# Kernel tuning notes

Hardware: AMD Instinct MI355X
Metric: run time of the kernel (lower is better)

Reference implementation:

```python
import jax, jax.numpy as jnp
import numpy as np

V, S, D, H = 32000, 1024, 768, 3072
EPS = 1e-5


def pos_encoding(seq_len, dim, dtype=jnp.float32):
    # pe[pos, i] = sin(pos/10000^(i/dim)) if i even else cos(pos/10000^(i/dim))
    pos = jnp.arange(seq_len, dtype=dtype)[:, None]
    i = jnp.arange(dim, dtype=dtype)[None, :]
    ang = pos / jnp.power(jnp.asarray(10000.0, dtype), i / dim)
    even = (jnp.arange(dim) % 2 == 0)[None, :]
    return jnp.where(even, jnp.sin(ang), jnp.cos(ang))


def layernorm2d(x, w, b):
    # normalizes over last two dims (token_size, input_dim), affine params [S, D]
    m = jnp.mean(x, axis=(-2, -1), keepdims=True)
    v = jnp.mean((x - m) ** 2, axis=(-2, -1), keepdims=True)
    return (x - m) / jnp.sqrt(v + EPS) * w + b


def setup_inputs() -> dict:
    key = jax.random.key(0)
    ks = jax.random.split(key, 16)
    sc = 0.02
    emb = jax.random.normal(ks[0], (V, D), jnp.float32) * sc
    emb = emb.at[0].set(0.0)  # padding_idx=0
    inp = {
        "x": jax.random.randint(ks[1], (8, S), 0, V),
        "emb": emb,
        "Wq": jax.random.normal(ks[2], (D, H), jnp.float32) * sc,
        "bq": jnp.zeros((H,), jnp.float32),
        "Wk": jax.random.normal(ks[3], (D, H), jnp.float32) * sc,
        "bk": jnp.zeros((H,), jnp.float32),
        "Wv": jax.random.normal(ks[4], (D, H), jnp.float32) * sc,
        "bv": jnp.zeros((H,), jnp.float32),
        "Wo": jax.random.normal(ks[5], (H, D), jnp.float32) * sc,
        "bo": jnp.zeros((D,), jnp.float32),
        "W1": jax.random.normal(ks[6], (D, H), jnp.float32) * sc,
        "b1": jnp.zeros((H,), jnp.float32),
        "W2": jax.random.normal(ks[7], (H, D), jnp.float32) * sc,
        "b2": jnp.zeros((D,), jnp.float32),
        "ln1_w": jnp.ones((S, D), jnp.float32),
        "ln1_b": jnp.zeros((S, D), jnp.float32),
        "ln2_w": jnp.ones((S, D), jnp.float32),
        "ln2_b": jnp.zeros((S, D), jnp.float32),
    }
    return inp


def reference(x, emb, Wq, bq, Wk, bk, Wv, bv, Wo, bo, W1, b1, W2, b2, ln1_w, ln1_b, ln2_w, ln2_b):
    y = emb[x]                                   # [B, S, D]
    y = y + pos_encoding(y.shape[1], y.shape[2], y.dtype)
    # unscaled self-attention (no 1/sqrt(d) factor, faithful to source)
    q = y @ Wq + bq
    k = y @ Wk + bk
    v = y @ Wv + bv
    attn = jax.nn.softmax(jnp.einsum("bsh,bth->bst", q, k), axis=-1)
    a = jnp.einsum("bst,bth->bsh", attn, v) @ Wo + bo
    y = layernorm2d(y + a, ln1_w, ln1_b)
    # FFN: GELU applied AFTER second linear (faithful to source)
    f = jax.nn.gelu((y @ W1 + b1) @ W2 + b2, approximate=False)
    y = layernorm2d(y + f, ln2_w, ln2_b)
    return y
```

## Files before the change

kernel.cpp:

```cpp
#include <hip/hip_runtime.h>
#include <hip/hip_fp16.h>

#define DI __device__ __forceinline__

typedef _Float16 f16x8 __attribute__((ext_vector_type(8)));
typedef float f32x4 __attribute__((ext_vector_type(4)));

struct alignas(8) h4 { __half x, y, z, w; };

DI float waveReduceSum(float v) {
#pragma unroll
  for (int i = 1; i < 64; i <<= 1) v += __shfl_xor(v, i);
  return v;
}
DI float waveReduceMax(float v) {
#pragma unroll
  for (int i = 1; i < 64; i <<= 1) v = fmaxf(v, __shfl_xor(v, i));
  return v;
}

DI float gelu_exact(float x) { return 0.5f * x * (1.f + erff(x * 0.70710678118654752f)); }

#define MFMA16(b_, a_, c_) __builtin_amdgcn_mfma_f32_16x16x32_f16((b_), (a_), (c_), 0, 0, 0)

template <typename CT, bool BIAS, bool BROW>
__global__ __launch_bounds__(512, 2) void gemm_nt8(
    const __half* __restrict__ A, int lda, long long sA,
    const __half* __restrict__ Bt, int ldb, long long sB,
    const float* __restrict__ bias, long long sBias,
    CT* __restrict__ C, int ldc, long long sC,
    int nT, int K) {
  __shared__ __align__(16) __half As[2][16384];
  __shared__ __align__(16) __half Bs[2][16384];

  const int tid = threadIdx.x;
  const int wave = tid >> 6, lane = tid & 63;

  const int gsz = 4 * nT;
  const int g = blockIdx.x / gsz, r = blockIdx.x % gsz;
  const int m0 = (g * 4 + (r & 3)) * 256;
  const int n0 = (r >> 2) * 256;

  A += (long long)blockIdx.z * sA;
  Bt += (long long)blockIdx.z * sB;
  C += (long long)blockIdx.z * sC;
  if constexpr (BIAS || BROW) bias += (long long)blockIdx.z * sBias;

  const int wm = wave >> 2, wn = wave & 3;

  f32x4 acc[8][4];
#pragma unroll
  for (int i = 0; i < 8; ++i)
#pragma unroll
    for (int j = 0; j < 4; ++j) acc[i][j] = (f32x4){0.f, 0.f, 0.f, 0.f};

  const int srow = tid >> 3;
  const int gc = (tid & 7) ^ (srow & 7);
  const __half* Ag = A + (size_t)(m0 + srow) * lda + gc * 8;
  const __half* Bg = Bt + (size_t)(n0 + srow) * ldb + gc * 8;
  const size_t a64 = (size_t)64 * lda, b64 = (size_t)64 * ldb;
  char* AsWr = (char*)As + tid * 16;
  char* BsWr = (char*)Bs + tid * 16;

  f16x8 sra[4], srb[4];

#define LDG(t)                                                        \
  {                                                                   \
    const __half* sa_ = Ag + (t) * 64;                                \
    const __half* sb_ = Bg + (t) * 64;                                \
    sra[0] = *(const f16x8*)(sa_);                                    \
    sra[1] = *(const f16x8*)(sa_ + a64);                              \
    sra[2] = *(const f16x8*)(sa_ + 2 * a64);                          \
    sra[3] = *(const f16x8*)(sa_ + 3 * a64);                          \
    srb[0] = *(const f16x8*)(sb_);                                    \
    srb[1] = *(const f16x8*)(sb_ + b64);                              \
    srb[2] = *(const f16x8*)(sb_ + 2 * b64);                          \
    srb[3] = *(const f16x8*)(sb_ + 3 * b64);                          \
  }
#define DSW(t)                                                        \
  {                                                                   \
    char* da_ = AsWr + (((t) & 1) ? 32768 : 0);                       \
    char* db_ = BsWr + (((t) & 1) ? 32768 : 0);                       \
    *(f16x8*)(da_) = sra[0];                                          \
    *(f16x8*)(da_ + 8192) = sra[1];                                   \
    *(f16x8*)(da_ + 16384) = sra[2];                                  \
    *(f16x8*)(da_ + 24576) = sra[3];                                  \
    *(f16x8*)(db_) = srb[0];                                          \
    *(f16x8*)(db_ + 8192) = srb[1];                                   \
    *(f16x8*)(db_ + 16384) = srb[2];                                  \
    *(f16x8*)(db_ + 24576) = srb[3];                                  \
  }

  const int ml = lane & 15, q = lane >> 4, lx = lane & 7;
  const int co0 = (q ^ lx) * 16, co1 = co0 ^ 64;
  const char* Ar = (const char*)As + wm * 16384 + ml * 128;
  const char* Br = (const char*)Bs + (wn >> 1) * 16384 + (wn & 1) * 8192 + ml * 128;

  const int nt = K >> 6;
  LDG(0);
  DSW(0);
  if (nt > 1) LDG(1);
  asm volatile("s_waitcnt lgkmcnt(0)" ::: "memory");
  __builtin_amdgcn_s_barrier();
  __builtin_amdgcn_sched_barrier(0);

  for (int t = 0; t < nt; ++t) {
    if (t + 1 < nt) {
      DSW(t + 1);
      if (t + 2 < nt) LDG(t + 2);
    }
    const int pb = (t & 1) ? 32768 : 0;
    const char* Ap = Ar + pb;
    const char* Bp = Br + pb;
    f16x8 af[8], bf[4];
#pragma unroll
    for (int ks = 0; ks < 2; ++ks) {
      const int co = ks ? co1 : co0;
#pragma unroll
      for (int i = 0; i < 8; ++i) af[i] = *(const f16x8*)(Ap + i * 2048 + co);
#pragma unroll
      for (int j = 0; j < 4; ++j) bf[j] = *(const f16x8*)(Bp + j * 2048 + co);
#pragma unroll
      for (int i = 0; i < 8; ++i)
#pragma unroll
        for (int j = 0; j < 4; ++j)
          acc[i][j] = MFMA16(bf[j], af[i], acc[i][j]);
    }
    asm volatile("s_waitcnt lgkmcnt(0)" ::: "memory");
    __builtin_amdgcn_s_barrier();
    __builtin_amdgcn_sched_barrier(0);
  }
#undef LDG
#undef DSW

#pragma unroll
  for (int j = 0; j < 4; ++j) {
    const int col0 = n0 + wn * 64 + j * 16 + q * 4;
    float4 bc = {0.f, 0.f, 0.f, 0.f};
    if constexpr (BIAS) bc = *(const float4*)(bias + col0);
#pragma unroll
    for (int i = 0; i < 8; ++i) {
      const int row = m0 + wm * 128 + i * 16 + ml;
      const float br = BROW ? bias[row] : 0.f;
      const float v0 = acc[i][j][0] + bc.x + br;
      const float v1 = acc[i][j][1] + bc.y + br;
      const float v2 = acc[i][j][2] + bc.z + br;
      const float v3 = acc[i][j][3] + bc.w + br;
      if constexpr (sizeof(CT) == 4) {
        *(float4*)(C + (size_t)row * ldc + col0) = make_float4(v0, v1, v2, v3);
      } else {
        h4 o{__float2half(v0), __float2half(v1), __float2half(v2), __float2half(v3)};
        *(h4*)((__half*)C + (size_t)row * ldc + col0) = o;
      }
    }
  }
}

template <typename CT, bool BIAS, bool BROW>
__global__ __launch_bounds__(256, 2) void gemm_nt(
    const __half* __restrict__ A, int lda, long long sA,
    const __half* __restrict__ Bt, int ldb, long long sB,
    const float* __restrict__ bias, long long sBias,
    CT* __restrict__ C, int ldc, long long sC,
    int nT, int K) {
  __shared__ __align__(16) __half As[2][8192];
  __shared__ __align__(16) __half Bs[2][8192];

  const int tid = threadIdx.x;
  const int wave = tid >> 6, lane = tid & 63;

  const int gsz = 8 * nT;
  const int g = blockIdx.x / gsz, r = blockIdx.x % gsz;
  const int m0 = (g * 8 + (r & 7)) * 128;
  const int n0 = (r >> 3) * 128;

  A += (long long)blockIdx.z * sA;
  Bt += (long long)blockIdx.z * sB;
  C += (long long)blockIdx.z * sC;
  if constexpr (BIAS || BROW) bias += (long long)blockIdx.z * sBias;
  const int wm = wave & 1, wn = wave >> 1;

  f32x4 acc[4][4];
#pragma unroll
  for (int i = 0; i < 4; ++i)
#pragma unroll
    for (int jj = 0; jj < 4; ++jj) acc[i][jj] = (f32x4){0.f, 0.f, 0.f, 0.f};

  const int srow = tid >> 3;
  const int gc = (tid & 7) ^ (srow & 7);
  const __half* Ag = A + (size_t)(m0 + srow) * lda + gc * 8;
  const __half* Bg = Bt + (size_t)(n0 + srow) * ldb + gc * 8;
  const size_t a32 = (size_t)32 * lda, b32 = (size_t)32 * ldb;
  char* AsWr = (char*)As + tid * 16;
  char* BsWr = (char*)Bs + tid * 16;

  f16x8 sra[4], srb[4];

#define LDG(t)                                                        \
  {                                                                   \
    const __half* sa_ = Ag + (t) * 64;                                \
    const __half* sb_ = Bg + (t) * 64;                                \
    sra[0] = *(const f16x8*)(sa_);                                    \
    sra[1] = *(const f16x8*)(sa_ + a32);                              \
    sra[2] = *(const f16x8*)(sa_ + 2 * a32);                          \
    sra[3] = *(const f16x8*)(sa_ + 3 * a32);                          \
    srb[0] = *(const f16x8*)(sb_);                                    \
    srb[1] = *(const f16x8*)(sb_ + b32);                              \
    srb[2] = *(const f16x8*)(sb_ + 2 * b32);                          \
    srb[3] = *(const f16x8*)(sb_ + 3 * b32);                          \
  }
#define DSW(t)                                                        \
  {                                                                   \
    char* da_ = AsWr + (((t) & 1) ? 16384 : 0);                       \
    char* db_ = BsWr + (((t) & 1) ? 16384 : 0);                       \
    *(f16x8*)(da_) = sra[0];                                          \
    *(f16x8*)(da_ + 4096) = sra[1];                                   \
    *(f16x8*)(da_ + 8192) = sra[2];                                   \
    *(f16x8*)(da_ + 12288) = sra[3];                                  \
    *(f16x8*)(db_) = srb[0];                                          \
    *(f16x8*)(db_ + 4096) = srb[1];                                   \
    *(f16x8*)(db_ + 8192) = srb[2];                                   \
    *(f16x8*)(db_ + 12288) = srb[3];                                  \
  }

  const int ml = lane & 15, q = lane >> 4, lx = lane & 7;
  const int aoff = ((wm * 64 + ml) * 8 + (q ^ lx)) * 16;
  const int boff = ((wn * 64 + ml) * 8 + (q ^ lx)) * 16;

  const int nt = K >> 6;
  LDG(0);
  DSW(0);
  if (nt > 1) LDG(1);
  asm volatile("s_waitcnt lgkmcnt(0)" ::: "memory");
  __builtin_amdgcn_s_barrier();
  __builtin_amdgcn_sched_barrier(0);

  for (int t = 0; t < nt; ++t) {
    if (t + 1 < nt) {
      DSW(t + 1);
      if (t + 2 < nt) LDG(t + 2);
    }
    const int pb = (t & 1) ? 16384 : 0;
#pragma unroll
    for (int jj = 0; jj < 2; ++jj) {
      const char* Ab = (const char*)As + pb + (jj ? (aoff ^ 64) : aoff);
      const char* Bb = (const char*)Bs + pb + (jj ? (boff ^ 64) : boff);
      f16x8 af[4], bf[4];
#pragma unroll
      for (int i = 0; i < 4; ++i) {
        af[i] = *(const f16x8*)(Ab + i * 2048);
        bf[i] = *(const f16x8*)(Bb + i * 2048);
      }
#pragma unroll
      for (int i = 0; i < 4; ++i)
#pragma unroll
        for (int jn = 0; jn < 4; ++jn)
          acc[i][jn] = MFMA16(bf[jn], af[i], acc[i][jn]);
    }
    asm volatile("s_waitcnt lgkmcnt(0)" ::: "memory");
    __builtin_amdgcn_s_barrier();
    __builtin_amdgcn_sched_barrier(0);
  }
#undef LDG
#undef DSW

#pragma unroll
  for (int jn = 0; jn < 4; ++jn) {
    const int col0 = n0 + wn * 64 + jn * 16 + q * 4;
    float4 bc = {0.f, 0.f, 0.f, 0.f};
    if constexpr (BIAS) bc = *(const float4*)(bias + col0);
#pragma unroll
    for (int i = 0; i < 4; ++i) {
      const int row = m0 + wm * 64 + i * 16 + ml;
      const float br = BROW ? bias[row] : 0.f;
      const float v0 = acc[i][jn][0] + bc.x + br;
      const float v1 = acc[i][jn][1] + bc.y + br;
      const float v2 = acc[i][jn][2] + bc.z + br;
      const float v3 = acc[i][jn][3] + bc.w + br;
      if constexpr (sizeof(CT) == 4) {
        *(float4*)(C + (size_t)row * ldc + col0) = make_float4(v0, v1, v2, v3);
      } else {
        h4 o{__float2half(v0), __float2half(v1), __float2half(v2), __float2half(v3)};
        *(h4*)((__half*)C + (size_t)row * ldc + col0) = o;
      }
    }
  }
}

__global__ __launch_bounds__(256) void prep(
    const float* __restrict__ Wq, const float* __restrict__ Wk,
    const float* __restrict__ Wv, const float* __restrict__ W1,
    const float* __restrict__ Wo, const float* __restrict__ W2,
    const float* __restrict__ bq, const float* __restrict__ bk,
    __half* __restrict__ wD, __half* __restrict__ wB, __half* __restrict__ wC,
    __half* __restrict__ wA, float* __restrict__ bqk) {
  if (blockIdx.x == 2304) {
    if (blockIdx.y == 0)
      for (int i = threadIdx.x; i < 3072; i += 256) {
        bqk[i] = bq[i];
        bqk[3072 + i] = bk[i];
      }
    return;
  }
  __shared__ float t[32][33];
  const int tx = threadIdx.x & 31, ty = threadIdx.x >> 5;
  if (blockIdx.y < 4) {
    const float* in;
    __half* out;
    switch (blockIdx.y) {
      case 0: in = Wq; out = wD; break;
      case 1: in = Wk; out = wD + 3072 * 768; break;
      case 2: in = Wv; out = wB; break;
      default: in = W1; out = wC; break;
    }
    const int cb = blockIdx.x % 96, rb = blockIdx.x / 96;
    const int c = cb * 32 + tx, r0 = rb * 32;
#pragma unroll
    for (int i = 0; i < 32; i += 8) t[ty + i][tx] = in[(size_t)(r0 + ty + i) * 3072 + c];
    __syncthreads();
    const int oc = r0 + tx, o0 = cb * 32;
#pragma unroll
    for (int i = 0; i < 32; i += 8)
      out[(size_t)(o0 + ty + i) * 768 + oc] = __float2half(t[tx][ty + i]);
  } else {
    const float* in = (blockIdx.y == 5) ? W2 : Wo;
    __half* out = wA + ((blockIdx.y == 5) ? 3072 * 768 : 0);
    const int cb = blockIdx.x % 24, rb = blockIdx.x / 24;
    const int c = cb * 32 + tx, r0 = rb * 32;
#pragma unroll
    for (int i = 0; i < 32; i += 8) t[ty + i][tx] = in[(size_t)(r0 + ty + i) * 768 + c];
    __syncthreads();
    const int oc = r0 + tx, o0 = cb * 32;
#pragma unroll
    for (int i = 0; i < 32; i += 8)
      out[(size_t)(o0 + ty + i) * 3072 + oc] = __float2half(t[tx][ty + i]);
  }
}

__global__ __launch_bounds__(256) void embed_pos_kernel(
    const int* __restrict__ x, const float* __restrict__ emb,
    float* __restrict__ y, __half* __restrict__ yh) {
  const int row = blockIdx.x;
  const int s = row & 1023;
  const int tok = x[row];
  const float* ep = emb + (size_t)tok * 768;
  float* yp = y + (size_t)row * 768;
  __half* hp = yh + (size_t)row * 768;
  const float c = -13.287712379549449f / 768.f;
  for (int d = threadIdx.x; d < 768; d += 256) {
    float ang = (float)s * exp2f((float)d * c);
    float pe = (d & 1) ? cosf(ang) : sinf(ang);
    float v = ep[d] + pe;
    yp[d] = v;
    hp[d] = __float2half(v);
  }
}

__global__ __launch_bounds__(256) void softmax_rows(
    const float* __restrict__ L, __half* __restrict__ P) {
  const size_t row = blockIdx.x;
  const float4 x = ((const float4*)(L + row * 1024))[threadIdx.x];
  const int wave = threadIdx.x >> 6, lane = threadIdx.x & 63;
  float m = fmaxf(fmaxf(x.x, x.y), fmaxf(x.z, x.w));
  m = waveReduceMax(m);
  __shared__ float sm[4];
  __shared__ float ssum[4];
  if (lane == 0) sm[wave] = m;
  __syncthreads();
  m = fmaxf(fmaxf(sm[0], sm[1]), fmaxf(sm[2], sm[3]));
  float e0 = expf(x.x - m), e1 = expf(x.y - m), e2 = expf(x.z - m), e3 = expf(x.w - m);
  float s = e0 + e1 + e2 + e3;
  s = waveReduceSum(s);
  if (lane == 0) ssum[wave] = s;
  __syncthreads();
  s = ssum[0] + ssum[1] + ssum[2] + ssum[3];
  const float inv = 1.f / s;
  h4 o{__float2half(e0 * inv), __float2half(e1 * inv), __float2half(e2 * inv),
       __float2half(e3 * inv)};
  ((h4*)(P + row * 1024))[threadIdx.x] = o;
}

template <bool GELU>
__global__ __launch_bounds__(256) void residual_stats(
    float* __restrict__ y, const float* __restrict__ p0, const float* __restrict__ p1,
    const float* __restrict__ bias, float2* __restrict__ partials) {
  const int b = blockIdx.y, chunk = blockIdx.x;
  const size_t base = (size_t)b * 786432 + (size_t)chunk * 8192;
  float4* yp = (float4*)(y + base);
  const float4* a0 = (const float4*)(p0 + base);
  const float4* a1 = (const float4*)(p1 + base);
  float s = 0.f, ss = 0.f;
#pragma unroll
  for (int it = 0; it < 8; ++it) {
    const int idx = it * 256 + threadIdx.x;
    const int d = (chunk * 8192 + it * 1024 + threadIdx.x * 4) % 768;
    float4 yv = yp[idx];
    float4 v0 = a0[idx];
    float4 v1 = a1[idx];
    const float4 bv = *(const float4*)(bias + d);
    float ax = v0.x + v1.x + bv.x, ay = v0.y + v1.y + bv.y;
    float az = v0.z + v1.z + bv.z, aw = v0.w + v1.w + bv.w;
    if constexpr (GELU) {
      ax = gelu_exact(ax); ay = gelu_exact(ay);
      az = gelu_exact(az); aw = gelu_exact(aw);
    }
    float4 r{yv.x + ax, yv.y + ay, yv.z + az, yv.w + aw};
    yp[idx] = r;
    s += r.x + r.y + r.z + r.w;
    ss += r.x * r.x + r.y * r.y + r.z * r.z + r.w * r.w;
  }
  s = waveReduceSum(s);
  ss = waveReduceSum(ss);
  __shared__ float2 wr[4];
  const int wave = threadIdx.x >> 6, lane = threadIdx.x & 63;
  if (lane == 0) wr[wave] = make_float2(s, ss);
  __syncthreads();
  if (threadIdx.x == 0) {
    float S = wr[0].x + wr[1].x + wr[2].x + wr[3].x;
    float SS = wr[0].y + wr[1].y + wr[2].y + wr[3].y;
    partials[b * 96 + chunk] = make_float2(S, SS);
  }
}

template <bool WB>
__global__ __launch_bounds__(256) void ln_apply(
    float* __restrict__ y, __half* __restrict__ yh, const float* __restrict__ w,
    const float* __restrict__ bb, const float2* __restrict__ partials) {
  const unsigned i4 = blockIdx.x * 256 + threadIdx.x;
  const unsigned i = i4 * 4;
  const unsigned b = i / 786432u;
  const int tid = threadIdx.x;
  float s = 0.f, ss = 0.f;
  if (tid < 96) {
    float2 p = partials[b * 96 + tid];
    s = p.x;
    ss = p.y;
  }
  s = waveReduceSum(s);
  ss = waveReduceSum(ss);
  __shared__ float2 wsum[4];
  if ((tid & 63) == 0) wsum[tid >> 6] = make_float2(s, ss);
  __syncthreads();
  const float S = wsum[0].x + wsum[1].x + wsum[2].x + wsum[3].x;
  const float SS = wsum[0].y + wsum[1].y + wsum[2].y + wsum[3].y;
  const float inv = 1.f / 786432.f;
  const float mean = S * inv;
  const float rstd = rsqrtf(SS * inv - mean * mean + 1e-5f);

  const unsigned e4 = (i - b * 786432u) >> 2;
  float4 yv = ((const float4*)y)[i4];
  const float4 wv = ((const float4*)w)[e4];
  const float4 bv = ((const float4*)bb)[e4];
  float4 r;
  r.x = (yv.x - mean) * rstd * wv.x + bv.x;
  r.y = (yv.y - mean) * rstd * wv.y + bv.y;
  r.z = (yv.z - mean) * rstd * wv.z + bv.z;
  r.w = (yv.w - mean) * rstd * wv.w + bv.w;
  ((float4*)y)[i4] = r;
  if constexpr (WB) {
    h4 o{__float2half(r.x), __float2half(r.y), __float2half(r.z), __float2half(r.w)};
    ((h4*)yh)[i4] = o;
  }
}

extern "C" void kernel_launch(void* const* d_in, const int* in_sizes, int n_in,
                              void* d_out, int out_size, void* d_ws, size_t ws_size,
                              hipStream_t stream) {
  const int* x = (const int*)d_in[0];
  const float* emb = (const float*)d_in[1];
  const float* Wq = (const float*)d_in[2];
  const float* bq = (const float*)d_in[3];
  const float* Wk = (const float*)d_in[4];
  const float* bk = (const float*)d_in[5];
  const float* Wv = (const float*)d_in[6];
  const float* bv = (const float*)d_in[7];
  const float* Wo = (const float*)d_in[8];
  const float* bo = (const float*)d_in[9];
  const float* W1 = (const float*)d_in[10];
  const float* b1 = (const float*)d_in[11];
  const float* W2 = (const float*)d_in[12];
  const float* b2 = (const float*)d_in[13];
  const float* ln1w = (const float*)d_in[14];
  const float* ln1b = (const float*)d_in[15];
  const float* ln2w = (const float*)d_in[16];
  const float* ln2b = (const float*)d_in[17];

  float* y = (float*)d_out;

  char* ws = (char*)d_ws;
  __half* yh = (__half*)(ws + 0);
  __half* qb = (__half*)(ws + 12582912);
  __half* kb = (__half*)(ws + 62914560);
  __half* Ph = kb;
  __half* vT = (__half*)(ws + 113246208);
  float* abuf = (float*)vT;
  float* Lg = (float*)(ws + 163577856);
  __half* wA = (__half*)(ws + 197132288);
  __half* wD = (__half*)(ws + 206569472);
  __half* wB = (__half*)(ws + 216006656);
  __half* wC = (__half*)(ws + 220725248);
  float* bqk = (float*)(ws + 225443840);
  float2* part = (float2*)(ws + 225468416);
  const size_t WS_NEEDED = 225474624;
  if (ws_size < WS_NEEDED) return;

  const dim3 blk(256), blk8(512);
  const long long SH = 1024LL * 3072, SS = 1024LL * 1024;
  const long long HALF = 25165824;
  float* p1 = abuf + 6291456;

  prep<<<dim3(2305, 6), blk, 0, stream>>>(Wq, Wk, Wv, W1, Wo, W2, bq, bk, wD, wB, wC, wA, bqk);
  embed_pos_kernel<<<dim3(8192), blk, 0, stream>>>(x, emb, y, yh);

  gemm_nt8<__half, true, false><<<dim3(384, 1, 2), blk8, 0, stream>>>(
      yh, 768, 0, wD, 768, 3072LL * 768, bqk, 3072, qb, 3072, HALF, 12, 768);

  gemm_nt<__half, false, true><<<dim3(192, 1, 8), blk, 0, stream>>>(
      wB, 768, 0, yh, 768, 1024LL * 768, bv, 0, vT, 1024, SH, 8, 768);

  gemm_nt<float, false, false><<<dim3(64, 1, 8), blk, 0, stream>>>(
      qb, 3072, SH, kb, 3072, SH, nullptr, 0, Lg, 1024, SS, 8, 3072);

  softmax_rows<<<dim3(8192), blk, 0, stream>>>(Lg, Ph);

  gemm_nt<__half, false, false><<<dim3(192, 1, 8), blk, 0, stream>>>(
      Ph, 1024, SS, vT, 1024, SH, nullptr, 0, (__half*)qb, 3072, SH, 24, 1024);

  gemm_nt<float, false, false><<<dim3(384, 1, 2), blk, 0, stream>>>(
      (__half*)qb, 3072, 1536, wA, 3072, 1536, nullptr, 0, abuf, 768, 6291456, 6, 1536);

  residual_stats<false><<<dim3(96, 8), blk, 0, stream>>>(y, abuf, p1, bo, part);
  ln_apply<true><<<dim3(6144), blk, 0, stream>>>(y, yh, ln1w, ln1b, part);

  gemm_nt<__half, true, false><<<dim3(1536, 1, 1), blk, 0, stream>>>(
      yh, 768, 0, wC, 768, 0, b1, 0, (__half*)qb, 3072, 0, 24, 768);
  gemm_nt<float, false, false><<<dim3(384, 1, 2), blk, 0, stream>>>(
      (__half*)qb, 3072, 1536, wA + 3072 * 768, 3072, 1536, nullptr, 0, abuf, 768, 6291456, 6, 1536);

  residual_stats<true><<<dim3(96, 8), blk, 0, stream>>>(y, abuf, p1, b2, part);
  ln_apply<false><<<dim3(6144), blk, 0, stream>>>(y, nullptr, ln2w, ln2b, part);
}
```

Baseline: 738.5 us.

## Single-buffer LDS in 128-tile GEMM and remap block IDs across XCDs

The 128x128 GEMM now uses a single LDS buffer instead of two, which halves its shared memory and raises the occupancy target to 3 blocks per CU. A global prefetch into registers still overlaps loads with compute. Both GEMM kernels also remap blockIdx so consecutive logical tiles land on the same XCD, which should improve L2 locality for the grouped tile order. The single buffer adds a barrier before each tile's LDS write and removes one stage of overlap. The remap also assumes gridDim.x is divisible by 8.

```diff
diff --git a/kernel.cpp b/kernel.cpp
--- a/kernel.cpp
+++ b/kernel.cpp
@@ -36,8 +36,11 @@
   const int tid = threadIdx.x;
   const int wave = tid >> 6, lane = tid & 63;
 
+  const int cpx = gridDim.x >> 3;
+  const int bid = (blockIdx.x & 7) * cpx + (blockIdx.x >> 3);
+
   const int gsz = 4 * nT;
-  const int g = blockIdx.x / gsz, r = blockIdx.x % gsz;
+  const int g = bid / gsz, r = bid % gsz;
   const int m0 = (g * 4 + (r & 3)) * 256;
   const int n0 = (r >> 2) * 256;
 
@@ -157,20 +160,23 @@
 }
 
 template <typename CT, bool BIAS, bool BROW>
-__global__ __launch_bounds__(256, 2) void gemm_nt(
+__global__ __launch_bounds__(256, 3) void gemm_nt(
     const __half* __restrict__ A, int lda, long long sA,
     const __half* __restrict__ Bt, int ldb, long long sB,
     const float* __restrict__ bias, long long sBias,
     CT* __restrict__ C, int ldc, long long sC,
     int nT, int K) {
-  __shared__ __align__(16) __half As[2][8192];
-  __shared__ __align__(16) __half Bs[2][8192];
+  __shared__ __align__(16) __half As[8192];
+  __shared__ __align__(16) __half Bs[8192];
 
   const int tid = threadIdx.x;
   const int wave = tid >> 6, lane = tid & 63;
 
+  const int cpx = gridDim.x >> 3;
+  const int bid = (blockIdx.x & 7) * cpx + (blockIdx.x >> 3);
+
   const int gsz = 8 * nT;
-  const int g = blockIdx.x / gsz, r = blockIdx.x % gsz;
+  const int g = bid / gsz, r = bid % gsz;
   const int m0 = (g * 8 + (r & 7)) * 128;
   const int n0 = (r >> 3) * 128;
 
@@ -209,18 +215,16 @@
     srb[2] = *(const f16x8*)(sb_ + 2 * b32);                          \
     srb[3] = *(const f16x8*)(sb_ + 3 * b32);                          \
   }
-#define DSW(t)                                                        \
+#define DSW()                                                         \
   {                                                                   \
-    char* da_ = AsWr + (((t) & 1) ? 16384 : 0);                       \
-    char* db_ = BsWr + (((t) & 1) ? 16384 : 0);                       \
-    *(f16x8*)(da_) = sra[0];                                          \
-    *(f16x8*)(da_ + 4096) = sra[1];                                   \
-    *(f16x8*)(da_ + 8192) = sra[2];                                   \
-    *(f16x8*)(da_ + 12288) = sra[3];                                  \
-    *(f16x8*)(db_) = srb[0];                                          \
-    *(f16x8*)(db_ + 4096) = srb[1];                                   \
-    *(f16x8*)(db_ + 8192) = srb[2];                                   \
-    *(f16x8*)(db_ + 12288) = srb[3];                                  \
+    *(f16x8*)(AsWr) = sra[0];                                         \
+    *(f16x8*)(AsWr + 4096) = sra[1];                                  \
+    *(f16x8*)(AsWr + 8192) = sra[2];                                  \
+    *(f16x8*)(AsWr + 12288) = sra[3];                                 \
+    *(f16x8*)(BsWr) = srb[0];                                         \
+    *(f16x8*)(BsWr + 4096) = srb[1];                                  \
+    *(f16x8*)(BsWr + 8192) = srb[2];                                  \
+    *(f16x8*)(BsWr + 12288) = srb[3];                                 \
   }
 
   const int ml = lane & 15, q = lane >> 4, lx = lane & 7;
@@ -229,22 +233,16 @@
 
   const int nt = K >> 6;
   LDG(0);
-  DSW(0);
-  if (nt > 1) LDG(1);
-  asm volatile("s_waitcnt lgkmcnt(0)" ::: "memory");
-  __builtin_amdgcn_s_barrier();
-  __builtin_amdgcn_sched_barrier(0);
-
   for (int t = 0; t < nt; ++t) {
-    if (t + 1 < nt) {
-      DSW(t + 1);
-      if (t + 2 < nt) LDG(t + 2);
-    }
-    const int pb = (t & 1) ? 16384 : 0;
+    DSW();
+    asm volatile("s_waitcnt lgkmcnt(0)" ::: "memory");
+    __builtin_amdgcn_s_barrier();
+    __builtin_amdgcn_sched_barrier(0);
+    if (t + 1 < nt) LDG(t + 1);
 #pragma unroll
     for (int jj = 0; jj < 2; ++jj) {
-      const char* Ab = (const char*)As + pb + (jj ? (aoff ^ 64) : aoff);
-      const char* Bb = (const char*)Bs + pb + (jj ? (boff ^ 64) : boff);
+      const char* Ab = (const char*)As + (jj ? (aoff ^ 64) : aoff);
+      const char* Bb = (const char*)Bs + (jj ? (boff ^ 64) : boff);
       f16x8 af[4], bf[4];
 #pragma unroll
       for (int i = 0; i < 4; ++i) {
```

New measurement: 741.5 us. About the same (+0.4%).
